# Kernel optimization log

Hardware: AMD Instinct MI355X
Metric: run time of the kernel (lower is better)

Reference implementation:

```python
import jax, jax.numpy as jnp
import numpy as np
import math

B, T, C, H, L, V = 16, 512, 1024, 16, 4, 32000
D = C // H


def setup_inputs() -> dict:
    key = jax.random.key(0)
    ks = jax.random.split(key, 10)
    X = jax.random.randint(ks[0], (B, T), 0, V)
    S = jax.random.bernoulli(ks[1], 0.5, (B, T)).astype(jnp.int32)
    # I + S must equal 1 everywhere, else get_attn_mask fully masks a row -> NaN softmax
    I = (1 - S).astype(jnp.float32)
    s = 0.02
    emb_table = jax.random.normal(ks[2], (V + 1, C), jnp.float32) * s
    pos_emb = jax.random.normal(ks[3], (T, C), jnp.float32) * s
    qkv_w = jax.random.normal(ks[4], (L, 3 * C, C), jnp.float32) * s
    out_w = jax.random.normal(ks[5], (L, C, C), jnp.float32) * s
    ffn_w1 = jax.random.normal(ks[6], (L, C, C), jnp.float32) * s
    ffn_b1 = jnp.zeros((L, C), jnp.float32)
    ffn_w2 = jax.random.normal(ks[7], (L, C, C), jnp.float32) * s
    ffn_b2 = jnp.zeros((L, C), jnp.float32)
    return dict(X=X, I=I, S=S, emb_table=emb_table, pos_emb=pos_emb,
                qkv_w=qkv_w, out_w=out_w, ffn_w1=ffn_w1, ffn_b1=ffn_b1,
                ffn_w2=ffn_w2, ffn_b2=ffn_b2)


def _forward(X, I, S, emb_table, pos_emb, qkv_w, out_w, ffn_w1, ffn_b1, ffn_w2, ffn_b2):
    # token_to_embeddings: unobserved (S==0) tokens remapped to sentinel index V
    Xm = X * S + (1 - S) * V                      # [B,T]
    x = emb_table[Xm] + pos_emb[None]             # [B,T,C]
    # additive mask from outer product of validity flags m = I + S
    m = I + S.astype(I.dtype)                     # [B,T]
    prod = m[:, :, None] * m[:, None, :]          # [B,T,T]
    bias = jnp.where(prod == 1.0, 0.0, -jnp.inf)[:, None]  # [B,1,T,T]
    scale = 1.0 / math.sqrt(D)
    for i in range(L):
        wq, wk, wv = qkv_w[i, :C], qkv_w[i, C:2 * C], qkv_w[i, 2 * C:]
        q = (x @ wq.T).reshape(B, T, H, D)
        k = (x @ wk.T).reshape(B, T, H, D)
        v = (x @ wv.T).reshape(B, T, H, D)
        scores = jnp.einsum('bqhd,bkhd->bhqk', q * scale, k) + bias
        attn = jax.nn.softmax(scores, axis=-1)
        o = jnp.einsum('bhqk,bkhd->bqhd', attn, v).reshape(B, T, C)
        x = o @ out_w[i].T + x                    # out projection + residual
        h = jax.nn.relu(x @ ffn_w1[i].T + ffn_b1[i])
        x = x + (h @ ffn_w2[i].T + ffn_b2[i])
    # readout: bmm(x^T, I) -> [B,C]
    return jnp.einsum('btc,bt->bc', x, I)


def reference(X, I, S, emb_table, pos_emb, qkv_w, out_w, ffn_w1, ffn_b1, ffn_w2, ffn_b2):
    return _forward(X, I, S, emb_table, pos_emb, qkv_w, out_w,
                    ffn_w1, ffn_b1, ffn_w2, ffn_b2)
```

## Files before the change

### kernel.cpp

```cpp
#include <hip/hip_runtime.h>
#include <stdint.h>

#define LAYERS 4
#define BB 16
#define TT 512
#define CC 1024
#define HH 16
#define DD 64
#define VV 32000
#define MM (BB*TT)

typedef __attribute__((ext_vector_type(8))) short bf16x8;
typedef __attribute__((ext_vector_type(4))) float f32x4;
typedef __attribute__((ext_vector_type(16))) float f32x16;

__device__ __forceinline__ unsigned short f2b(float f) {
  union { float f; unsigned int u; } v; v.f = f;
  unsigned int r = v.u + 0x7FFFu + ((v.u >> 16) & 1u);
  return (unsigned short)(r >> 16);
}
__device__ __forceinline__ float blo(unsigned int u) {
  union { unsigned int x; float f; } v; v.x = u << 16; return v.f;
}
__device__ __forceinline__ float bhi(unsigned int u) {
  union { unsigned int x; float f; } v; v.x = u & 0xFFFF0000u; return v.f;
}
__device__ __forceinline__ uint32_t pkbf(float lo, float hi) {
  uint32_t d; asm("v_cvt_pk_bf16_f32 %0, %1, %2" : "=v"(d) : "v"(lo), "v"(hi)); return d;
}
__device__ __forceinline__ float ex2(float x) {
  float r; asm("v_exp_f32 %0, %1" : "=v"(r) : "v"(x)); return r;
}
__device__ __forceinline__ void gload16(const unsigned short* g, const unsigned short* lds) {
  __builtin_amdgcn_global_load_lds((const __attribute__((address_space(1))) void*)g,
                                   (__attribute__((address_space(3))) void*)lds, 16, 0, 0);
}

__global__ __launch_bounds__(256) void cvt_kernel(const float* __restrict__ src,
                                                  unsigned short* __restrict__ dst, int n4) {
  int i = blockIdx.x * 256 + threadIdx.x;
  if (i >= n4) return;
  float4 v = ((const float4*)src)[i];
  ushort4 o; o.x = f2b(v.x); o.y = f2b(v.y); o.z = f2b(v.z); o.w = f2b(v.w);
  ((ushort4*)dst)[i] = o;
}

__global__ __launch_bounds__(256) void embed_kernel(const int* __restrict__ X, const int* __restrict__ S,
    const float* __restrict__ emb, const float* __restrict__ pos,
    float* __restrict__ x, unsigned short* __restrict__ xb) {
  int bt = blockIdx.x; int tid = threadIdx.x;
  int t = bt & (TT - 1);
  int tok = S[bt] ? X[bt] : VV;
  float4 e = ((const float4*)(emb + (size_t)tok * CC))[tid];
  float4 p = ((const float4*)(pos + (size_t)t * CC))[tid];
  float4 r; r.x = e.x + p.x; r.y = e.y + p.y; r.z = e.z + p.z; r.w = e.w + p.w;
  ((float4*)(x + (size_t)bt * CC))[tid] = r;
  ushort4 ub; ub.x = f2b(r.x); ub.y = f2b(r.y); ub.z = f2b(r.z); ub.w = f2b(r.w);
  ((ushort4*)(xb + (size_t)bt * CC))[tid] = ub;
}

template<int EPI, int BM>
__global__ __launch_bounds__(512, 4) void gemm8_kernel(
    const unsigned short* __restrict__ A,
    const unsigned short* __restrict__ W,
    float* __restrict__ xres,
    unsigned short* __restrict__ outb,
    const float* __restrict__ bias,
    int N, int nbx) {
  constexpr int NA = BM / 128;
  constexpr int MI = BM / 64;
  constexpr int BUFS = (BM + 128) * 32;
  extern __shared__ unsigned short lds[];
  const int K = 1024;
  const int tid = threadIdx.x;
  const int wv = tid >> 6, ln = tid & 63;
  const int g = ln >> 4, rr = ln & 15;
  const int wm = wv >> 1, wn = wv & 1;

  const int nwg = gridDim.x;
  const int bid = blockIdx.x;
  const int swz = (bid & 7) * (nwg >> 3) + (bid >> 3);
  const int by = swz / nbx, bx = swz - by * nbx;
  const int brow = by * BM, bcol = bx * 128;

  const unsigned short* asrc[NA];
  #pragma unroll
  for (int rd = 0; rd < NA; ++rd) {
    int p = rd * 512 + tid;
    int row = p >> 2, gg = p & 3;
    asrc[rd] = A + (size_t)(brow + row) * K + (gg ^ ((row >> 1) & 3)) * 8;
  }
  const unsigned short* bsrc;
  {
    int row = tid >> 2, gg = tid & 3;
    bsrc = W + (size_t)(bcol + row) * K + (gg ^ ((row >> 1) & 3)) * 8;
  }

  auto stage = [&](int tile, int buf) {
    unsigned short* Aba = lds + buf * BUFS;
    unsigned short* Bba = Aba + BM * 32;
    int ko = tile * 32;
    #pragma unroll
    for (int rd = 0; rd < NA; ++rd)
      gload16(asrc[rd] + ko, Aba + (rd * 512 + wv * 64) * 8);
    gload16(bsrc + ko, Bba + (wv * 64) * 8);
  };

  f32x4 acc[MI][4];
  #pragma unroll
  for (int i = 0; i < MI; ++i)
    #pragma unroll
    for (int j = 0; j < 4; ++j)
      acc[i][j] = (f32x4){0.f, 0.f, 0.f, 0.f};

  stage(0, 0);

  const int chx = (g ^ ((rr >> 1) & 3)) * 8;
  for (int t = 0; t < 32; ++t) {
    if (t < 31) {
      stage(t + 1, (t + 1) & 1);
      asm volatile("s_waitcnt vmcnt(%0)" :: "i"(NA + 1) : "memory");
    } else {
      asm volatile("s_waitcnt vmcnt(0)" ::: "memory");
    }
    __builtin_amdgcn_s_barrier();
    __builtin_amdgcn_sched_barrier(0);

    const unsigned short* Aba = lds + (t & 1) * BUFS;
    const unsigned short* Bba = Aba + BM * 32;
    bf16x8 av[MI], bv[4];
    #pragma unroll
    for (int i = 0; i < MI; ++i)
      av[i] = *(const bf16x8*)(Aba + (wm * (BM / 4) + i * 16 + rr) * 32 + chx);
    #pragma unroll
    for (int j = 0; j < 4; ++j)
      bv[j] = *(const bf16x8*)(Bba + (wn * 64 + j * 16 + rr) * 32 + chx);

    __builtin_amdgcn_s_setprio(1);
    #pragma unroll
    for (int i = 0; i < MI; ++i)
      #pragma unroll
      for (int j = 0; j < 4; ++j)
        acc[i][j] = __builtin_amdgcn_mfma_f32_16x16x32_bf16(av[i], bv[j], acc[i][j], 0, 0, 0);
    __builtin_amdgcn_s_setprio(0);
    __builtin_amdgcn_sched_barrier(0);
    __builtin_amdgcn_s_barrier();
  }

  #pragma unroll
  for (int i = 0; i < MI; ++i) {
    #pragma unroll
    for (int j = 0; j < 4; ++j) {
      #pragma unroll
      for (int q = 0; q < 4; ++q) {
        int rowg = brow + wm * (BM / 4) + i * 16 + g * 4 + q;
        int colg = bcol + wn * 64 + j * 16 + rr;
        size_t off = (size_t)rowg * N + colg;
        float vacc = acc[i][j][q];
        if (EPI == 0) {
          outb[off] = f2b(vacc);
        } else if (EPI == 1) {
          float nx = xres[off] + vacc;
          xres[off] = nx; outb[off] = f2b(nx);
        } else if (EPI == 2) {
          float hv = vacc + bias[colg];
          hv = hv > 0.f ? hv : 0.f;
          outb[off] = f2b(hv);
        } else {
          float nx = xres[off] + vacc + bias[colg];
          xres[off] = nx; outb[off] = f2b(nx);
        }
      }
    }
  }
}

template<int E>
__device__ __forceinline__ bf16x8 buildP(const f32x16& p) {
  uint32_t a = pkbf(p[E + 0], p[E + 1]);
  uint32_t b = pkbf(p[E + 4], p[E + 5]);
  uint32_t c = pkbf(p[E + 2], p[E + 3]);
  uint32_t d = pkbf(p[E + 6], p[E + 7]);
  asm("v_permlane32_swap_b32 %0, %1" : "+v"(a), "+v"(b));
  asm("v_permlane32_swap_b32 %0, %1" : "+v"(c), "+v"(d));
  union { uint32_t u[4]; bf16x8 v; } r;
  r.u[0] = a; r.u[1] = c; r.u[2] = b; r.u[3] = d;
  return r.v;
}

__global__ __launch_bounds__(256) void attn_kernel(const unsigned short* __restrict__ qkv,
                                                   unsigned short* __restrict__ ob) {
  __shared__ unsigned short Kl[64 * 64];
  __shared__ unsigned short Vt[64 * 64];
  const int tid = threadIdx.x;
  const int wv = tid >> 6, ln = tid & 63;
  const int lq = ln & 31, hi = ln >> 5;
  const int qt = blockIdx.x >> 8, bh = blockIdx.x & 255;
  const int b = bh >> 4, h = bh & 15;
  const int qrow = qt * 128 + wv * 32 + lq;
  const size_t rowQ = (size_t)(b * TT + qrow) * 3072 + h * 64;

  const float cs = 0.125f * 1.44269504f;
  bf16x8 qf[4];
  #pragma unroll
  for (int t = 0; t < 4; ++t) {
    uint4 u = *(const uint4*)(qkv + rowQ + t * 16 + hi * 8);
    uint32_t w[4] = {u.x, u.y, u.z, u.w};
    union { uint32_t u4[4]; bf16x8 v; } cv;
    #pragma unroll
    for (int j = 0; j < 4; ++j) cv.u4[j] = pkbf(blo(w[j]) * cs, bhi(w[j]) * cs);
    qf[t] = cv.v;
  }

  f32x16 o0 = {}, o1 = {};
  float mrun = -3.0e38f, lsum = 0.f;

  for (int kv0 = 0; kv0 < TT; kv0 += 64) {
    if (kv0) __syncthreads();
    #pragma unroll
    for (int r = 0; r < 2; ++r) {
      int ch = r * 256 + tid;
      int k = ch >> 3, cc = ch & 7;
      int sg = (k & 7) ^ (k >> 3);
      const unsigned short* gs = qkv + (size_t)(b * TT + kv0 + k) * 3072 + 1024 + h * 64 + ((cc ^ sg) << 3);
      gload16(gs, Kl + (size_t)(r * 256 + wv * 64) * 8);
    }
    {
      int cc = tid & 7, kp = tid >> 3;
      int k = kp * 2;
      const unsigned short* gv = qkv + (size_t)(b * TT + kv0 + k) * 3072 + 2048 + h * 64 + cc * 8;
      uint4 g1 = *(const uint4*)gv;
      uint4 g2 = *(const uint4*)(gv + 3072);
      uint32_t w1[4] = {g1.x, g1.y, g1.z, g1.w}, w2[4] = {g2.x, g2.y, g2.z, g2.w};
      #pragma unroll
      for (int j = 0; j < 8; ++j) {
        int d = cc * 8 + j;
        uint32_t dw = (j & 1) ? ((w1[j >> 1] >> 16) | (w2[j >> 1] & 0xFFFF0000u))
                              : ((w1[j >> 1] & 0xFFFFu) | (w2[j >> 1] << 16));
        int sg = (d & 7) ^ (d >> 3);
        *(uint32_t*)(Vt + d * 64 + (k ^ (sg << 3))) = dw;
      }
    }
    __syncthreads();

    f32x16 s0 = {}, s1 = {};
    #pragma unroll
    for (int t = 0; t < 4; ++t) {
      int r0 = lq, r1 = 32 + lq;
      bf16x8 a0 = *(const bf16x8*)(Kl + r0 * 64 + ((((t << 1) | hi) ^ ((r0 & 7) ^ (r0 >> 3))) << 3));
      bf16x8 a1 = *(const bf16x8*)(Kl + r1 * 64 + ((((t << 1) | hi) ^ ((r1 & 7) ^ (r1 >> 3))) << 3));
      s0 = __builtin_amdgcn_mfma_f32_32x32x16_bf16(a0, qf[t], s0, 0, 0, 0);
      s1 = __builtin_amdgcn_mfma_f32_32x32x16_bf16(a1, qf[t], s1, 0, 0, 0);
    }

    float mx = s0[0];
    #pragma unroll
    for (int r = 1; r < 16; ++r) mx = fmaxf(mx, s0[r]);
    #pragma unroll
    for (int r = 0; r < 16; ++r) mx = fmaxf(mx, s1[r]);
    mx = fmaxf(mx, __shfl_xor(mx, 32));
    float mnew = fmaxf(mrun, mx);
    float cf = ex2(mrun - mnew);
    mrun = mnew;
    lsum *= cf;
    #pragma unroll
    for (int r = 0; r < 16; ++r) { o0[r] *= cf; o1[r] *= cf; }
    #pragma unroll
    for (int r = 0; r < 16; ++r) {
      s0[r] = ex2(s0[r] - mnew);
      s1[r] = ex2(s1[r] - mnew);
      lsum += s0[r] + s1[r];
    }

    bf16x8 pf0 = buildP<0>(s0);
    bf16x8 pf1 = buildP<8>(s0);
    bf16x8 pf2 = buildP<0>(s1);
    bf16x8 pf3 = buildP<8>(s1);

    #pragma unroll
    for (int t = 0; t < 4; ++t) {
      bf16x8 pf = (t == 0) ? pf0 : (t == 1) ? pf1 : (t == 2) ? pf2 : pf3;
      int d0 = lq, d1 = 32 + lq;
      bf16x8 v0 = *(const bf16x8*)(Vt + d0 * 64 + ((((t << 1) | hi) ^ ((d0 & 7) ^ (d0 >> 3))) << 3));
      bf16x8 v1 = *(const bf16x8*)(Vt + d1 * 64 + ((((t << 1) | hi) ^ ((d1 & 7) ^ (d1 >> 3))) << 3));
      o0 = __builtin_amdgcn_mfma_f32_32x32x16_bf16(v0, pf, o0, 0, 0, 0);
      o1 = __builtin_amdgcn_mfma_f32_32x32x16_bf16(v1, pf, o1, 0, 0, 0);
    }
  }

  lsum += __shfl_xor(lsum, 32);
  float inv = 1.f / lsum;
  size_t orow = (size_t)(b * TT + qrow) * CC + h * 64;
  #pragma unroll
  for (int md = 0; md < 2; ++md) {
    #pragma unroll
    for (int rq = 0; rq < 4; ++rq) {
      int d0 = md * 32 + rq * 8 + hi * 4;
      float e0 = (md ? o1[rq * 4 + 0] : o0[rq * 4 + 0]) * inv;
      float e1 = (md ? o1[rq * 4 + 1] : o0[rq * 4 + 1]) * inv;
      float e2 = (md ? o1[rq * 4 + 2] : o0[rq * 4 + 2]) * inv;
      float e3 = (md ? o1[rq * 4 + 3] : o0[rq * 4 + 3]) * inv;
      uint2 st; st.x = pkbf(e0, e1); st.y = pkbf(e2, e3);
      *(uint2*)(ob + orow + d0) = st;
    }
  }
}

__global__ __launch_bounds__(256) void final_kernel(const float* __restrict__ x,
                                                    const float* __restrict__ I,
                                                    float* __restrict__ out) {
  int b = blockIdx.x >> 2;
  int c = ((blockIdx.x & 3) << 8) + threadIdx.x;
  float acc = 0.f;
  const float* xp = x + (size_t)b * TT * CC + c;
  const float* Ip = I + (size_t)b * TT;
  for (int t = 0; t < TT; ++t) acc = fmaf(xp[(size_t)t * CC], Ip[t], acc);
  out[b * CC + c] = acc;
}

extern "C" void kernel_launch(void* const* d_in, const int* in_sizes, int n_in,
                              void* d_out, int out_size, void* d_ws, size_t ws_size,
                              hipStream_t stream) {
  const int*   X      = (const int*)d_in[0];
  const float* I      = (const float*)d_in[1];
  const int*   S      = (const int*)d_in[2];
  const float* emb    = (const float*)d_in[3];
  const float* pos    = (const float*)d_in[4];
  const float* qkv_w  = (const float*)d_in[5];
  const float* out_w  = (const float*)d_in[6];
  const float* ffn_w1 = (const float*)d_in[7];
  const float* ffn_b1 = (const float*)d_in[8];
  const float* ffn_w2 = (const float*)d_in[9];
  const float* ffn_b2 = (const float*)d_in[10];
  float* out = (float*)d_out;

  char* ws = (char*)d_ws;
  size_t off = 0;
  auto walloc = [&](size_t bytes) { char* p = ws + off; off += (bytes + 255) & ~(size_t)255; return p; };
  unsigned short* wqkv = (unsigned short*)walloc((size_t)LAYERS * 3 * CC * CC * 2);
  unsigned short* wo   = (unsigned short*)walloc((size_t)LAYERS * CC * CC * 2);
  unsigned short* w1   = (unsigned short*)walloc((size_t)LAYERS * CC * CC * 2);
  unsigned short* w2   = (unsigned short*)walloc((size_t)LAYERS * CC * CC * 2);
  float*          x    = (float*)walloc((size_t)MM * CC * 4);
  unsigned short* xb   = (unsigned short*)walloc((size_t)MM * CC * 2);
  unsigned short* qkvb = (unsigned short*)walloc((size_t)MM * 3 * CC * 2);
  unsigned short* obuf = (unsigned short*)walloc((size_t)MM * CC * 2);
  unsigned short* hbuf = (unsigned short*)walloc((size_t)MM * CC * 2);
  if (off > ws_size) return;

  int n4;
  n4 = LAYERS * 3 * CC * CC / 4; cvt_kernel<<<(n4 + 255) / 256, 256, 0, stream>>>(qkv_w, wqkv, n4);
  n4 = LAYERS * CC * CC / 4;     cvt_kernel<<<(n4 + 255) / 256, 256, 0, stream>>>(out_w, wo, n4);
  n4 = LAYERS * CC * CC / 4;     cvt_kernel<<<(n4 + 255) / 256, 256, 0, stream>>>(ffn_w1, w1, n4);
  n4 = LAYERS * CC * CC / 4;     cvt_kernel<<<(n4 + 255) / 256, 256, 0, stream>>>(ffn_w2, w2, n4);

  embed_kernel<<<MM, 256, 0, stream>>>(X, S, emb, pos, x, xb);

  const size_t lds256 = 2 * (256 + 128) * 32 * 2;
  const size_t lds128 = 2 * (128 + 128) * 32 * 2;
  for (int l = 0; l < LAYERS; ++l) {
    gemm8_kernel<0, 256><<<(MM / 256) * (3 * CC / 128), 512, lds256, stream>>>(
        xb, wqkv + (size_t)l * 3 * CC * CC, nullptr, qkvb, nullptr, 3 * CC, 3 * CC / 128);
    attn_kernel<<<4 * 256, 256, 0, stream>>>(qkvb, obuf);
    gemm8_kernel<1, 128><<<(MM / 128) * (CC / 128), 512, lds128, stream>>>(
        obuf, wo + (size_t)l * CC * CC, x, xb, nullptr, CC, CC / 128);
    gemm8_kernel<2, 128><<<(MM / 128) * (CC / 128), 512, lds128, stream>>>(
        xb, w1 + (size_t)l * CC * CC, nullptr, hbuf, ffn_b1 + l * CC, CC, CC / 128);
    gemm8_kernel<3, 128><<<(MM / 128) * (CC / 128), 512, lds128, stream>>>(
        hbuf, w2 + (size_t)l * CC * CC, x, xb, ffn_b2 + l * CC, CC, CC / 128);
  }

  final_kernel<<<BB * 4, 256, 0, stream>>>(x, I, out);
}
```

Before: 779.9 us.

## Double-buffer K/V tiles in attention, prefetch next tile, and rescale lazily

The attention kernel now keeps two LDS buffers for K and transposed V. It issues the loads for the next 64-key tile before computing on the current one, so global memory latency overlaps the MFMA work and one barrier per iteration is removed. The online softmax only rescales the output accumulators when the running max grows by more than a threshold, and it uses a tree max reduction. MFMA sections also run at raised wave priority. This doubles LDS use and relies on ordering of waitcnt and barriers for correctness.

After: 778.9 us. No clear change (-0.1%).

```diff
diff --git a/kernel.cpp b/kernel.cpp
--- a/kernel.cpp
+++ b/kernel.cpp
@@ -190,8 +190,8 @@
 
 __global__ __launch_bounds__(256) void attn_kernel(const unsigned short* __restrict__ qkv,
                                                    unsigned short* __restrict__ ob) {
-  __shared__ unsigned short Kl[64 * 64];
-  __shared__ unsigned short Vt[64 * 64];
+  __shared__ unsigned short Kl[2][64 * 64];
+  __shared__ unsigned short Vt[2][64 * 64];
   const int tid = threadIdx.x;
   const int wv = tid >> 6, ln = tid & 63;
   const int lq = ln & 31, hi = ln >> 5;
@@ -212,63 +212,84 @@
     qf[t] = cv.v;
   }
 
-  f32x16 o0 = {}, o1 = {};
-  float mrun = -3.0e38f, lsum = 0.f;
-
-  for (int kv0 = 0; kv0 < TT; kv0 += 64) {
-    if (kv0) __syncthreads();
+  auto stageK = [&](int i, int p) {
     #pragma unroll
     for (int r = 0; r < 2; ++r) {
       int ch = r * 256 + tid;
       int k = ch >> 3, cc = ch & 7;
       int sg = (k & 7) ^ (k >> 3);
-      const unsigned short* gs = qkv + (size_t)(b * TT + kv0 + k) * 3072 + 1024 + h * 64 + ((cc ^ sg) << 3);
-      gload16(gs, Kl + (size_t)(r * 256 + wv * 64) * 8);
-    }
-    {
-      int cc = tid & 7, kp = tid >> 3;
-      int k = kp * 2;
-      const unsigned short* gv = qkv + (size_t)(b * TT + kv0 + k) * 3072 + 2048 + h * 64 + cc * 8;
-      uint4 g1 = *(const uint4*)gv;
-      uint4 g2 = *(const uint4*)(gv + 3072);
-      uint32_t w1[4] = {g1.x, g1.y, g1.z, g1.w}, w2[4] = {g2.x, g2.y, g2.z, g2.w};
-      #pragma unroll
-      for (int j = 0; j < 8; ++j) {
-        int d = cc * 8 + j;
-        uint32_t dw = (j & 1) ? ((w1[j >> 1] >> 16) | (w2[j >> 1] & 0xFFFF0000u))
-                              : ((w1[j >> 1] & 0xFFFFu) | (w2[j >> 1] << 16));
-        int sg = (d & 7) ^ (d >> 3);
-        *(uint32_t*)(Vt + d * 64 + (k ^ (sg << 3))) = dw;
-      }
-    }
-    __syncthreads();
+      const unsigned short* gs = qkv + (size_t)(b * TT + i * 64 + k) * 3072 + 1024 + h * 64 + ((cc ^ sg) << 3);
+      gload16(gs, &Kl[p][(size_t)(r * 256 + wv * 64) * 8]);
+    }
+  };
+  auto loadV = [&](int i, uint4& g1, uint4& g2) {
+    int cc = tid & 7, kp = tid >> 3;
+    const unsigned short* gv = qkv + (size_t)(b * TT + i * 64 + kp * 2) * 3072 + 2048 + h * 64 + cc * 8;
+    g1 = *(const uint4*)gv;
+    g2 = *(const uint4*)(gv + 3072);
+  };
+  auto writeVt = [&](int p, uint4 g1, uint4 g2) {
+    int cc = tid & 7, k = (tid >> 3) * 2;
+    uint32_t w1[4] = {g1.x, g1.y, g1.z, g1.w}, w2[4] = {g2.x, g2.y, g2.z, g2.w};
+    #pragma unroll
+    for (int j = 0; j < 8; ++j) {
+      int d = cc * 8 + j;
+      uint32_t dw = (j & 1) ? ((w1[j >> 1] >> 16) | (w2[j >> 1] & 0xFFFF0000u))
+                            : ((w1[j >> 1] & 0xFFFFu) | (w2[j >> 1] << 16));
+      int sg = (d & 7) ^ (d >> 3);
+      *(uint32_t*)(&Vt[p][d * 64 + (k ^ (sg << 3))]) = dw;
+    }
+  };
+
+  f32x16 o0 = {}, o1 = {};
+  float mrun = -3.0e38f, lsum = 0.f;
+
+  uint4 vg1, vg2;
+  stageK(0, 0);
+  loadV(0, vg1, vg2);
+  writeVt(0, vg1, vg2);
+  asm volatile("s_waitcnt lgkmcnt(0)" ::: "memory");
+  __builtin_amdgcn_s_barrier();
+
+  for (int i = 0; i < 8; ++i) {
+    const int p = i & 1;
+    if (i < 7) { stageK(i + 1, p ^ 1); loadV(i + 1, vg1, vg2); }
 
     f32x16 s0 = {}, s1 = {};
+    __builtin_amdgcn_s_setprio(1);
     #pragma unroll
     for (int t = 0; t < 4; ++t) {
       int r0 = lq, r1 = 32 + lq;
-      bf16x8 a0 = *(const bf16x8*)(Kl + r0 * 64 + ((((t << 1) | hi) ^ ((r0 & 7) ^ (r0 >> 3))) << 3));
-      bf16x8 a1 = *(const bf16x8*)(Kl + r1 * 64 + ((((t << 1) | hi) ^ ((r1 & 7) ^ (r1 >> 3))) << 3));
+      bf16x8 a0 = *(const bf16x8*)(&Kl[p][r0 * 64 + ((((t << 1) | hi) ^ ((r0 & 7) ^ (r0 >> 3))) << 3)]);
+      bf16x8 a1 = *(const bf16x8*)(&Kl[p][r1 * 64 + ((((t << 1) | hi) ^ ((r1 & 7) ^ (r1 >> 3))) << 3)]);
       s0 = __builtin_amdgcn_mfma_f32_32x32x16_bf16(a0, qf[t], s0, 0, 0, 0);
       s1 = __builtin_amdgcn_mfma_f32_32x32x16_bf16(a1, qf[t], s1, 0, 0, 0);
     }
-
-    float mx = s0[0];
-    #pragma unroll
-    for (int r = 1; r < 16; ++r) mx = fmaxf(mx, s0[r]);
-    #pragma unroll
-    for (int r = 0; r < 16; ++r) mx = fmaxf(mx, s1[r]);
-    mx = fmaxf(mx, __shfl_xor(mx, 32));
-    float mnew = fmaxf(mrun, mx);
-    float cf = ex2(mrun - mnew);
-    mrun = mnew;
-    lsum *= cf;
-    #pragma unroll
-    for (int r = 0; r < 16; ++r) { o0[r] *= cf; o1[r] *= cf; }
+    __builtin_amdgcn_s_setprio(0);
+
+    float m8[8];
+    #pragma unroll
+    for (int r = 0; r < 8; ++r)
+      m8[r] = fmaxf(fmaxf(s0[r], s0[r + 8]), fmaxf(s1[r], s1[r + 8]));
+    #pragma unroll
+    for (int st = 4; st > 0; st >>= 1)
+      #pragma unroll
+      for (int r = 0; r < st; ++r)
+        m8[r] = fmaxf(m8[r], m8[r + st]);
+    float mx = fmaxf(m8[0], __shfl_xor(m8[0], 32));
+
+    if (!__all(mx - mrun <= 8.0f)) {
+      float mnew = fmaxf(mrun, mx);
+      float cf = ex2(mrun - mnew);
+      lsum *= cf;
+      #pragma unroll
+      for (int r = 0; r < 16; ++r) { o0[r] *= cf; o1[r] *= cf; }
+      mrun = mnew;
+    }
     #pragma unroll
     for (int r = 0; r < 16; ++r) {
-      s0[r] = ex2(s0[r] - mnew);
-      s1[r] = ex2(s1[r] - mnew);
+      s0[r] = ex2(s0[r] - mrun);
+      s1[r] = ex2(s1[r] - mrun);
       lsum += s0[r] + s1[r];
     }
 
@@ -277,15 +298,23 @@
     bf16x8 pf2 = buildP<0>(s1);
     bf16x8 pf3 = buildP<8>(s1);
 
+    if (i < 7) writeVt(p ^ 1, vg1, vg2);
+
+    __builtin_amdgcn_s_setprio(1);
     #pragma unroll
     for (int t = 0; t < 4; ++t) {
       bf16x8 pf = (t == 0) ? pf0 : (t == 1) ? pf1 : (t == 2) ? pf2 : pf3;
       int d0 = lq, d1 = 32 + lq;
-      bf16x8 v0 = *(const bf16x8*)(Vt + d0 * 64 + ((((t << 1) | hi) ^ ((d0 & 7) ^ (d0 >> 3))) << 3));
-      bf16x8 v1 = *(const bf16x8*)(Vt + d1 * 64 + ((((t << 1) | hi) ^ ((d1 & 7) ^ (d1 >> 3))) << 3));
+      bf16x8 v0 = *(const bf16x8*)(&Vt[p][d0 * 64 + ((((t << 1) | hi) ^ ((d0 & 7) ^ (d0 >> 3))) << 3)]);
+      bf16x8 v1 = *(const bf16x8*)(&Vt[p][d1 * 64 + ((((t << 1) | hi) ^ ((d1 & 7) ^ (d1 >> 3))) << 3)]);
       o0 = __builtin_amdgcn_mfma_f32_32x32x16_bf16(v0, pf, o0, 0, 0, 0);
       o1 = __builtin_amdgcn_mfma_f32_32x32x16_bf16(v1, pf, o1, 0, 0, 0);
     }
+    __builtin_amdgcn_s_setprio(0);
+
+    asm volatile("s_waitcnt lgkmcnt(0)" ::: "memory");
+    __builtin_amdgcn_sched_barrier(0);
+    __builtin_amdgcn_s_barrier();
   }
 
   lsum += __shfl_xor(lsum, 32);
```
